# Kernel tuning notes

Hardware: AMD Instinct MI355X
Metric: run time of the kernel (lower is better)

## Reference

```python
import jax, jax.numpy as jnp
import numpy as np

D_MODEL = 1024
H = 16
D_K = D_MODEL // H


def setup_inputs() -> dict:
    key = jax.random.key(0)
    ks = jax.random.split(key, 11)
    B, S = 4, 2048
    q = jax.random.normal(ks[0], (B, S, D_MODEL), dtype=jnp.float32)
    k = jax.random.normal(ks[1], (B, S, D_MODEL), dtype=jnp.float32)
    v = jax.random.normal(ks[2], (B, S, D_MODEL), dtype=jnp.float32)
    mask = jnp.ones((1, 1, S, S), dtype=bool)  # all-ones = no masking
    scale = 1.0 / np.sqrt(D_MODEL)
    wq = jax.random.normal(ks[3], (D_MODEL, D_MODEL), dtype=jnp.float32) * scale
    wk = jax.random.normal(ks[4], (D_MODEL, D_MODEL), dtype=jnp.float32) * scale
    wv = jax.random.normal(ks[5], (D_MODEL, D_MODEL), dtype=jnp.float32) * scale
    wo = jax.random.normal(ks[6], (D_MODEL, D_MODEL), dtype=jnp.float32) * scale
    bq = jnp.zeros((D_MODEL,), jnp.float32)
    bk = jnp.zeros((D_MODEL,), jnp.float32)
    bv = jnp.zeros((D_MODEL,), jnp.float32)
    bo = jnp.zeros((D_MODEL,), jnp.float32)
    return {"q": q, "k": k, "v": v, "mask": mask,
            "wq": wq, "bq": bq, "wk": wk, "bk": bk,
            "wv": wv, "bv": bv, "wo": wo, "bo": bo}


def reference(q, k, v, mask, wq, bq, wk, bk, wv, bv, wo, bo):
    B, S, _ = q.shape
    # projections (Linear uses x @ W^T + b)
    qh = (q @ wq.T + bq).reshape(B, S, H, D_K).transpose(0, 2, 1, 3)  # [B,H,S,Dk]
    kh = (k @ wk.T + bk).reshape(B, S, H, D_K).transpose(0, 2, 1, 3)
    vh = (v @ wv.T + bv).reshape(B, S, H, D_K).transpose(0, 2, 1, 3)
    scores = jnp.einsum("bhqd,bhkd->bhqk", qh, kh) / jnp.sqrt(jnp.float32(D_K))
    scores = jnp.where(mask, scores, jnp.float32(-1e9))
    attn = jax.nn.softmax(scores, axis=-1)  # dropout p=0.0 -> identity
    out = jnp.einsum("bhqk,bhkd->bhqd", attn, vh)  # [B,H,S,Dk]
    out = out.transpose(0, 2, 1, 3).reshape(B, S, D_MODEL)
    return out @ wo.T + bo
```

## Files before the change

### kernel.cpp

```cpp
#include <hip/hip_runtime.h>
#include <hip/hip_bf16.h>


typedef __attribute__((ext_vector_type(8))) short bf16x8;
typedef __attribute__((ext_vector_type(4))) float f32x4;
typedef __attribute__((ext_vector_type(16))) float f32x16;

__device__ __forceinline__ float fast_exp2(float x) {
  return __builtin_amdgcn_exp2f(x);
}

__device__ __forceinline__ void gload_lds16(const void* g, void* l) {
  __builtin_amdgcn_global_load_lds(
      (const __attribute__((address_space(1))) unsigned int*)g,
      (__attribute__((address_space(3))) unsigned int*)l, 16, 0, 0);
}

__global__ void cvt_bf16_all(const float* __restrict__ s0, const float* __restrict__ s1,
                             const float* __restrict__ s2, const float* __restrict__ s3,
                             const float* __restrict__ s4, const float* __restrict__ s5,
                             const float* __restrict__ s6,
                             __hip_bfloat16* __restrict__ d0, __hip_bfloat16* __restrict__ d1,
                             __hip_bfloat16* __restrict__ d2, __hip_bfloat16* __restrict__ d3,
                             __hip_bfloat16* __restrict__ d4, __hip_bfloat16* __restrict__ d5,
                             __hip_bfloat16* __restrict__ d6,
                             int nw4, int nx4) {
  const int z = blockIdx.y;
  const float* in;
  __hip_bfloat16* out;
  int n4;
  switch (z) {
    case 0: in = s0; out = d0; n4 = nw4; break;
    case 1: in = s1; out = d1; n4 = nw4; break;
    case 2: in = s2; out = d2; n4 = nw4; break;
    case 3: in = s3; out = d3; n4 = nw4; break;
    case 4: in = s4; out = d4; n4 = nx4; break;
    case 5: in = s5; out = d5; n4 = nx4; break;
    default: in = s6; out = d6; n4 = nx4; break;
  }
  int stride = gridDim.x * blockDim.x;
  for (int i = blockIdx.x * blockDim.x + threadIdx.x; i < n4; i += stride) {
    float4 f = reinterpret_cast<const float4*>(in)[i];
    union { __hip_bfloat16 h[4]; ushort4 u; } cv;
    cv.h[0] = __float2bfloat16(f.x);
    cv.h[1] = __float2bfloat16(f.y);
    cv.h[2] = __float2bfloat16(f.z);
    cv.h[3] = __float2bfloat16(f.w);
    reinterpret_cast<ushort4*>(out)[i] = cv.u;
  }
}

template <int MODE>
__device__ __forceinline__ void gemm_tile(const __hip_bfloat16* __restrict__ A,
                                          const __hip_bfloat16* __restrict__ W,
                                          const float* __restrict__ bias,
                                          void* __restrict__ out, float scale,
                                          int m0, int n0,
                                          __hip_bfloat16* As, __hip_bfloat16* Bs) {
  const int t = threadIdx.x;
  const int lane = t & 63;
  const int w = t >> 6;
  const int lrow = lane & 15, lk = lane >> 4;
  const int wr = (w >> 1) << 6;
  const int wc = (w & 1) << 6;
  const int K = 1024, N = 1024;

  f32x4 acc[4][4] = {};
  const char* Ab = (const char*)As;
  const char* Bb = (const char*)Bs;

  for (int kt = 0; kt < K; kt += 64) {
    #pragma unroll
    for (int j = 0; j < 4; ++j) {
      int i = j * 256 + t;
      int row = i >> 3;
      int cs = ((i & 7) ^ (row & 7)) << 3;
      gload_lds16(A + (size_t)(m0 + row) * K + kt + cs, (char*)As + (i << 4));
      gload_lds16(W + (size_t)(n0 + row) * K + kt + cs, (char*)Bs + (i << 4));
    }
    __syncthreads();
    #pragma unroll
    for (int h = 0; h < 2; ++h) {
      bf16x8 a[4], b[4];
      #pragma unroll
      for (int f = 0; f < 4; ++f) {
        const int sw = ((h * 4 + lk) ^ (lrow & 7)) << 4;
        a[f] = *(const bf16x8*)(Ab + (wr + f * 16 + lrow) * 128 + sw);
        b[f] = *(const bf16x8*)(Bb + (wc + f * 16 + lrow) * 128 + sw);
      }
      #pragma unroll
      for (int fi = 0; fi < 4; ++fi)
        #pragma unroll
        for (int fj = 0; fj < 4; ++fj)
          acc[fi][fj] = __builtin_amdgcn_mfma_f32_16x16x32_bf16(a[fi], b[fj], acc[fi][fj], 0, 0, 0);
    }
    __syncthreads();
  }

  #pragma unroll
  for (int fi = 0; fi < 4; ++fi) {
    int rbase = m0 + wr + fi * 16 + (lk << 2);
    #pragma unroll
    for (int fj = 0; fj < 4; ++fj) {
      int gc = n0 + wc + fj * 16 + lrow;
      float bv = bias[gc];
      #pragma unroll
      for (int r = 0; r < 4; ++r) {
        int gm = rbase + r;
        float val = (acc[fi][fj][r] + bv) * scale;
        if (MODE == 0) {
          int bb = gm >> 11, ss = gm & 2047, hh = gc >> 6, dd = gc & 63;
          ((__hip_bfloat16*)out)[((((size_t)bb * 16 + hh) * 2048 + ss) << 6) + dd] =
              __float2bfloat16(val);
        } else {
          ((float*)out)[(size_t)gm * N + gc] = val;
        }
      }
    }
  }
}

__global__ __launch_bounds__(256, 3)
void gemm_qkv_kernel(const __hip_bfloat16* __restrict__ A0, const __hip_bfloat16* __restrict__ A1,
                     const __hip_bfloat16* __restrict__ A2,
                     const __hip_bfloat16* __restrict__ W0, const __hip_bfloat16* __restrict__ W1,
                     const __hip_bfloat16* __restrict__ W2,
                     const float* __restrict__ b0, const float* __restrict__ b1,
                     const float* __restrict__ b2,
                     __hip_bfloat16* __restrict__ o0, __hip_bfloat16* __restrict__ o1,
                     __hip_bfloat16* __restrict__ o2,
                     float sc0, float sc1, float sc2) {
  __shared__ __hip_bfloat16 As[128 * 64];
  __shared__ __hip_bfloat16 Bs[128 * 64];
  const int flat = blockIdx.x;
  const int swz = (flat & 7) * 192 + (flat >> 3);
  const int z = swz >> 9;
  const int rem = swz & 511;
  const int m0 = (rem >> 3) << 7;
  const int n0 = (rem & 7) << 7;
  const __hip_bfloat16* A = A0; const __hip_bfloat16* W = W0;
  const float* bias = b0; __hip_bfloat16* out = o0; float scale = sc0;
  if (z == 1) { A = A1; W = W1; bias = b1; out = o1; scale = sc1; }
  else if (z == 2) { A = A2; W = W2; bias = b2; out = o2; scale = sc2; }
  gemm_tile<0>(A, W, bias, out, scale, m0, n0, As, Bs);
}

__global__ __launch_bounds__(256, 3)
void gemm_out_kernel(const __hip_bfloat16* __restrict__ A, const __hip_bfloat16* __restrict__ W,
                     const float* __restrict__ bias, float* __restrict__ out) {
  __shared__ __hip_bfloat16 As[128 * 64];
  __shared__ __hip_bfloat16 Bs[128 * 64];
  const int flat = blockIdx.x;
  const int swz = (flat & 7) * 64 + (flat >> 3);
  const int m0 = (swz >> 3) << 7;
  const int n0 = (swz & 7) << 7;
  gemm_tile<1>(A, W, bias, out, 1.0f, m0, n0, As, Bs);
}


template <int OFF>
__device__ __forceinline__ bf16x8 pack8(const f32x16& v) {
  bf16x8 r;
  #pragma unroll
  for (int e = 0; e < 8; ++e) {
    union { __hip_bfloat16 h; short s; } u;
    u.h = __float2bfloat16(v[OFF + e]);
    r[e] = u.s;
  }
  return r;
}

__global__ __launch_bounds__(512, 4)
void attn32_kernel(const __hip_bfloat16* __restrict__ qh,
                   const __hip_bfloat16* __restrict__ kh,
                   const __hip_bfloat16* __restrict__ vh,
                   __hip_bfloat16* __restrict__ att) {
  const int t = threadIdx.x;
  const int lane = t & 63, w = t >> 6;
  const int l31 = lane & 31, g = lane >> 5;
  const int bh = blockIdx.x, q0 = blockIdx.y << 8;

  const __hip_bfloat16* Qp = qh + (size_t)bh * 2048 * 64;
  const __hip_bfloat16* Kp = kh + (size_t)bh * 2048 * 64;
  const __hip_bfloat16* Vp = vh + (size_t)bh * 2048 * 64;

  __shared__ __align__(16) char lds[4 * 8192 + 4 * 9216];
  char* const Vbase = lds + 4 * 8192;

  const int qrow = q0 + w * 32 + l31;
  bf16x8 bq[4];
  #pragma unroll
  for (int ks = 0; ks < 4; ++ks)
    bq[ks] = *(const bf16x8*)(Qp + (size_t)qrow * 64 + ks * 16 + g * 8);

  bf16x8 ones;
  #pragma unroll
  for (int e = 0; e < 8; ++e) ones[e] = (short)0x3F80;

  f32x16 o0 = {}, o1 = {}, lacc = {};

  const int krow = t >> 3, kcc = t & 7;
  const size_t kgo = (size_t)krow * 64 + ((kcc ^ (krow & 7)) << 3);
  const int klo = t << 4;
  const int vkey = t & 63, vdb = (t >> 6) << 3;
  const size_t vgo = (size_t)vkey * 64 + vdb;
  const int kpos = (vkey & 0x30) | (vkey & 3) | ((vkey & 4) << 1) | ((vkey & 8) >> 1);
  int ka[4], kb_[4], va_[4], vb_[4];
  #pragma unroll
  for (int ks = 0; ks < 4; ++ks) {
    ka[ks] = l31 * 128 + (((ks * 2 + g) ^ (l31 & 7)) << 4);
    kb_[ks] = ka[ks] + 32 * 128;
  }
  #pragma unroll
  for (int st = 0; st < 4; ++st) {
    va_[st] = l31 * 144 + st * 32 + g * 16;
    vb_[st] = va_[st] + 32 * 144;
  }

  auto vwrite = [&](char* Vn, const bf16x8& v) {
    #pragma unroll
    for (int e = 0; e < 8; ++e)
      *(unsigned short*)(Vn + (vdb + e) * 144 + kpos * 2) = (unsigned short)v[e];
  };

  auto subtile = [&](const char* Kc, const char* Vc) {
    f32x16 s0 = {}, s1 = {};
    __builtin_amdgcn_s_setprio(1);
    #pragma unroll
    for (int ks = 0; ks < 4; ++ks) {
      bf16x8 a0 = *(const bf16x8*)(Kc + ka[ks]);
      bf16x8 a1 = *(const bf16x8*)(Kc + kb_[ks]);
      s0 = __builtin_amdgcn_mfma_f32_32x32x16_bf16(a0, bq[ks], s0, 0, 0, 0);
      s1 = __builtin_amdgcn_mfma_f32_32x32x16_bf16(a1, bq[ks], s1, 0, 0, 0);
    }
    __builtin_amdgcn_s_setprio(0);

    #pragma unroll
    for (int j = 0; j < 16; ++j) {
      s0[j] = fast_exp2(s0[j]);
      s1[j] = fast_exp2(s1[j]);
    }

    bf16x8 pb0 = pack8<0>(s0), pb1 = pack8<8>(s0);
    bf16x8 pb2 = pack8<0>(s1), pb3 = pack8<8>(s1);

    __builtin_amdgcn_s_setprio(1);
    #pragma unroll
    for (int st = 0; st < 4; ++st) {
      bf16x8 av0 = *(const bf16x8*)(Vc + va_[st]);
      bf16x8 av1 = *(const bf16x8*)(Vc + vb_[st]);
      const bf16x8 pb = (st == 0) ? pb0 : (st == 1) ? pb1 : (st == 2) ? pb2 : pb3;
      o0 = __builtin_amdgcn_mfma_f32_32x32x16_bf16(av0, pb, o0, 0, 0, 0);
      o1 = __builtin_amdgcn_mfma_f32_32x32x16_bf16(av1, pb, o1, 0, 0, 0);
      lacc = __builtin_amdgcn_mfma_f32_32x32x16_bf16(ones, pb, lacc, 0, 0, 0);
    }
    __builtin_amdgcn_s_setprio(0);
  };

  {
    #pragma unroll
    for (int s = 0; s < 2; ++s) {
      gload_lds16(Kp + s * 4096 + kgo, lds + s * 8192 + klo);
      bf16x8 v0 = *(const bf16x8*)(Vp + s * 4096 + vgo);
      vwrite(Vbase + s * 9216, v0);
    }
  }
  __syncthreads();

  for (int it = 0; it < 16; ++it) {
    const int P = it & 1;
    const char* Kc0 = lds + (P * 2) * 8192;
    const char* Kc1 = Kc0 + 8192;
    const char* Vc0 = Vbase + (P * 2) * 9216;
    const char* Vc1 = Vc0 + 9216;
    char* Kn0 = lds + ((P ^ 1) * 2) * 8192;
    char* Vn0 = Vbase + ((P ^ 1) * 2) * 9216;

    bf16x8 vrA, vrB;
    const bool pre = (it < 15);
    if (pre) {
      const size_t nb = (size_t)(it + 1) * 8192;
      gload_lds16(Kp + nb + kgo, Kn0 + klo);
      gload_lds16(Kp + nb + 4096 + kgo, Kn0 + 8192 + klo);
      vrA = *(const bf16x8*)(Vp + nb + vgo);
      vrB = *(const bf16x8*)(Vp + nb + 4096 + vgo);
    }

    subtile(Kc0, Vc0);
    subtile(Kc1, Vc1);

    if (pre) {
      vwrite(Vn0, vrA);
      vwrite(Vn0 + 9216, vrB);
    }
    __syncthreads();
  }

  const int bb = bh >> 4, hh = bh & 15;
  const float inv = 1.f / lacc[0];
  __hip_bfloat16* obase = att + ((size_t)bb * 2048 + qrow) * 1024 + hh * 64 + g * 16;

  auto epi = [&](const f32x16& acc, __hip_bfloat16* dst) {
    float fin[16];
    #pragma unroll
    for (int c2 = 0; c2 < 2; ++c2)
      #pragma unroll
      for (int c4 = 0; c4 < 4; ++c4) {
        float sendv = g ? acc[c4 + 4 * c2] : acc[c4 + 4 * (2 + c2)];
        float recvv = __shfl_xor(sendv, 32);
        float ownv  = g ? acc[c4 + 4 * (2 + c2)] : acc[c4 + 4 * c2];
        fin[c2 * 8 + c4]     = g ? recvv : ownv;
        fin[c2 * 8 + 4 + c4] = g ? ownv : recvv;
      }
    bf16x8 w0, w1;
    #pragma unroll
    for (int j = 0; j < 8; ++j) {
      union { __hip_bfloat16 h; short s; } u0, u1;
      u0.h = __float2bfloat16(fin[j] * inv);
      u1.h = __float2bfloat16(fin[8 + j] * inv);
      w0[j] = u0.s; w1[j] = u1.s;
    }
    *(bf16x8*)dst = w0;
    *(bf16x8*)(dst + 8) = w1;
  };
  epi(o0, obase);
  epi(o1, obase + 32);
}

extern "C" void kernel_launch(void* const* d_in, const int* in_sizes, int n_in,
                              void* d_out, int out_size, void* d_ws, size_t ws_size,
                              hipStream_t stream) {
  (void)in_sizes; (void)n_in; (void)out_size; (void)ws_size;
  const float* q  = (const float*)d_in[0];
  const float* k  = (const float*)d_in[1];
  const float* v  = (const float*)d_in[2];
  const float* wq = (const float*)d_in[4];
  const float* bq = (const float*)d_in[5];
  const float* wk = (const float*)d_in[6];
  const float* bk = (const float*)d_in[7];
  const float* wv = (const float*)d_in[8];
  const float* bv = (const float*)d_in[9];
  const float* wo = (const float*)d_in[10];
  const float* bo = (const float*)d_in[11];

  char* ws = (char*)d_ws;
  const size_t MB = 1u << 20;
  __hip_bfloat16* wqb  = (__hip_bfloat16*)(ws);
  __hip_bfloat16* wkb  = (__hip_bfloat16*)(ws + 2 * MB);
  __hip_bfloat16* wvb  = (__hip_bfloat16*)(ws + 4 * MB);
  __hip_bfloat16* wob  = (__hip_bfloat16*)(ws + 6 * MB);
  __hip_bfloat16* qb   = (__hip_bfloat16*)(ws + 8 * MB);
  __hip_bfloat16* kb   = (__hip_bfloat16*)(ws + 24 * MB);
  __hip_bfloat16* vb   = (__hip_bfloat16*)(ws + 40 * MB);
  __hip_bfloat16* qhb  = (__hip_bfloat16*)(ws + 56 * MB);
  __hip_bfloat16* khb  = (__hip_bfloat16*)(ws + 72 * MB);
  __hip_bfloat16* vhb  = (__hip_bfloat16*)(ws + 88 * MB);
  __hip_bfloat16* attb = qb;

  dim3 blk(256);
  const int nw4 = (1024 * 1024) / 4;
  const int nx4 = (4 * 2048 * 1024) / 4;
  const float qscale = 0.125f * 1.44269504f;

  cvt_bf16_all<<<dim3(1024, 7), blk, 0, stream>>>(wq, wk, wv, wo, q, k, v,
                                                  wqb, wkb, wvb, wob, qb, kb, vb,
                                                  nw4, nx4);

  gemm_qkv_kernel<<<dim3(1536), blk, 0, stream>>>(qb, kb, vb, wqb, wkb, wvb,
                                                  bq, bk, bv, qhb, khb, vhb,
                                                  qscale, 1.0f, 1.0f);

  attn32_kernel<<<dim3(64, 8), dim3(512), 0, stream>>>(qhb, khb, vhb, attb);

  gemm_out_kernel<<<dim3(512), blk, 0, stream>>>(attb, wob, bo, (float*)d_out);
}
```

Before: 190.7 us.

## Compute softmax row sums with VALU adds and pack V transpose writes as dwords

Drops the third MFMA per step that multiplied P by a ones vector to get the softmax denominator. The row sum is now built from the exp values with scalar adds and one cross-half shuffle, cutting matrix-core work by about a third in the PV phase. The V transpose into LDS is also rearranged: each thread loads two adjacent key rows of four dims and writes packed 32-bit words, replacing eight 16-bit stores. The conversion kernel grid is doubled as well. Summing in fp32 before bf16 packing changes rounding slightly.

```diff
diff --git a/kernel.cpp b/kernel.cpp
--- a/kernel.cpp
+++ b/kernel.cpp
@@ -193,18 +193,16 @@
   for (int ks = 0; ks < 4; ++ks)
     bq[ks] = *(const bf16x8*)(Qp + (size_t)qrow * 64 + ks * 16 + g * 8);
 
-  bf16x8 ones;
-  #pragma unroll
-  for (int e = 0; e < 8; ++e) ones[e] = (short)0x3F80;
-
-  f32x16 o0 = {}, o1 = {}, lacc = {};
+  f32x16 o0 = {}, o1 = {};
+  float l_run = 0.f;
 
   const int krow = t >> 3, kcc = t & 7;
   const size_t kgo = (size_t)krow * 64 + ((kcc ^ (krow & 7)) << 3);
   const int klo = t << 4;
-  const int vkey = t & 63, vdb = (t >> 6) << 3;
-  const size_t vgo = (size_t)vkey * 64 + vdb;
-  const int kpos = (vkey & 0x30) | (vkey & 3) | ((vkey & 4) << 1) | ((vkey & 8) >> 1);
+  const int vp = t & 31;
+  const int vdb = (t >> 5) << 2;
+  const int k2 = vp << 1;
+  const int kpos = (k2 & 0x30) | (k2 & 3) | ((k2 & 4) << 1) | ((k2 & 8) >> 1);
   int ka[4], kb_[4], va_[4], vb_[4];
   #pragma unroll
   for (int ks = 0; ks < 4; ++ks) {
@@ -217,10 +215,15 @@
     vb_[st] = va_[st] + 32 * 144;
   }
 
-  auto vwrite = [&](char* Vn, const bf16x8& v) {
-    #pragma unroll
-    for (int e = 0; e < 8; ++e)
-      *(unsigned short*)(Vn + (vdb + e) * 144 + kpos * 2) = (unsigned short)v[e];
+  auto vwrite = [&](char* Vn, const ushort4& va, const ushort4& vb) {
+    unsigned int u0 = (unsigned int)va.x | ((unsigned int)vb.x << 16);
+    unsigned int u1 = (unsigned int)va.y | ((unsigned int)vb.y << 16);
+    unsigned int u2 = (unsigned int)va.z | ((unsigned int)vb.z << 16);
+    unsigned int u3 = (unsigned int)va.w | ((unsigned int)vb.w << 16);
+    *(unsigned int*)(Vn + (vdb + 0) * 144 + kpos * 2) = u0;
+    *(unsigned int*)(Vn + (vdb + 1) * 144 + kpos * 2) = u1;
+    *(unsigned int*)(Vn + (vdb + 2) * 144 + kpos * 2) = u2;
+    *(unsigned int*)(Vn + (vdb + 3) * 144 + kpos * 2) = u3;
   };
 
   auto subtile = [&](const char* Kc, const char* Vc) {
@@ -240,6 +243,12 @@
       s0[j] = fast_exp2(s0[j]);
       s1[j] = fast_exp2(s1[j]);
     }
+    float as[8];
+    #pragma unroll
+    for (int j = 0; j < 8; ++j) as[j] = (s0[j] + s0[j + 8]) + (s1[j] + s1[j + 8]);
+    float ps = ((as[0] + as[1]) + (as[2] + as[3])) + ((as[4] + as[5]) + (as[6] + as[7]));
+    ps += __shfl_xor(ps, 32);
+    l_run += ps;
 
     bf16x8 pb0 = pack8<0>(s0), pb1 = pack8<8>(s0);
     bf16x8 pb2 = pack8<0>(s1), pb3 = pack8<8>(s1);
@@ -252,7 +261,6 @@
       const bf16x8 pb = (st == 0) ? pb0 : (st == 1) ? pb1 : (st == 2) ? pb2 : pb3;
       o0 = __builtin_amdgcn_mfma_f32_32x32x16_bf16(av0, pb, o0, 0, 0, 0);
       o1 = __builtin_amdgcn_mfma_f32_32x32x16_bf16(av1, pb, o1, 0, 0, 0);
-      lacc = __builtin_amdgcn_mfma_f32_32x32x16_bf16(ones, pb, lacc, 0, 0, 0);
     }
     __builtin_amdgcn_s_setprio(0);
   };
@@ -261,8 +269,9 @@
     #pragma unroll
     for (int s = 0; s < 2; ++s) {
       gload_lds16(Kp + s * 4096 + kgo, lds + s * 8192 + klo);
-      bf16x8 v0 = *(const bf16x8*)(Vp + s * 4096 + vgo);
-      vwrite(Vbase + s * 9216, v0);
+      ushort4 va = *(const ushort4*)(Vp + (size_t)(s * 64 + k2) * 64 + vdb);
+      ushort4 vb = *(const ushort4*)(Vp + (size_t)(s * 64 + k2 + 1) * 64 + vdb);
+      vwrite(Vbase + s * 9216, va, vb);
     }
   }
   __syncthreads();
@@ -276,28 +285,30 @@
     char* Kn0 = lds + ((P ^ 1) * 2) * 8192;
     char* Vn0 = Vbase + ((P ^ 1) * 2) * 9216;
 
-    bf16x8 vrA, vrB;
+    ushort4 vrA0, vrA1, vrB0, vrB1;
     const bool pre = (it < 15);
     if (pre) {
-      const size_t nb = (size_t)(it + 1) * 8192;
-      gload_lds16(Kp + nb + kgo, Kn0 + klo);
-      gload_lds16(Kp + nb + 4096 + kgo, Kn0 + 8192 + klo);
-      vrA = *(const bf16x8*)(Vp + nb + vgo);
-      vrB = *(const bf16x8*)(Vp + nb + 4096 + vgo);
+      const size_t nb = (size_t)(it + 1) * 128;
+      gload_lds16(Kp + nb * 64 + kgo, Kn0 + klo);
+      gload_lds16(Kp + (nb + 64) * 64 + kgo, Kn0 + 8192 + klo);
+      vrA0 = *(const ushort4*)(Vp + (nb + k2) * 64 + vdb);
+      vrA1 = *(const ushort4*)(Vp + (nb + k2 + 1) * 64 + vdb);
+      vrB0 = *(const ushort4*)(Vp + (nb + 64 + k2) * 64 + vdb);
+      vrB1 = *(const ushort4*)(Vp + (nb + 64 + k2 + 1) * 64 + vdb);
     }
 
     subtile(Kc0, Vc0);
     subtile(Kc1, Vc1);
 
     if (pre) {
-      vwrite(Vn0, vrA);
-      vwrite(Vn0 + 9216, vrB);
+      vwrite(Vn0, vrA0, vrA1);
+      vwrite(Vn0 + 9216, vrB0, vrB1);
     }
     __syncthreads();
   }
 
   const int bb = bh >> 4, hh = bh & 15;
-  const float inv = 1.f / lacc[0];
+  const float inv = 1.f / l_run;
   __hip_bfloat16* obase = att + ((size_t)bb * 2048 + qrow) * 1024 + hh * 64 + g * 16;
 
   auto epi = [&](const f32x16& acc, __hip_bfloat16* dst) {
@@ -362,7 +373,7 @@
   const int nx4 = (4 * 2048 * 1024) / 4;
   const float qscale = 0.125f * 1.44269504f;
 
-  cvt_bf16_all<<<dim3(1024, 7), blk, 0, stream>>>(wq, wk, wv, wo, q, k, v,
+  cvt_bf16_all<<<dim3(2048, 7), blk, 0, stream>>>(wq, wk, wv, wo, q, k, v,
                                                   wqb, wkb, wvb, wob, qb, kb, vb,
                                                   nw4, nx4);
 
```

After: 204.0 us. +7.0%, slower.
